# Kernel optimization log

Measured on AMD Instinct MI355X. Metric: run time of the kernel, lower is better.

## Reference

```python
import jax, jax.numpy as jnp
import numpy as np

D_MODEL = 768
D_INNER = 1536
D_STATE = 16
D_CONV = 4
DT_RANK = 48
N_LAYER = 4
VOCAB = 32000
B, L = 2, 1024


def rmsnorm(x, w, eps=1e-5):
    return x * jax.lax.rsqrt(jnp.mean(x * x, axis=-1, keepdims=True) + eps) * w


def depthwise_causal_conv(u, w):
    # u: (b, l, d_in), w: (d_in, k). torch pads both sides then truncates to l,
    # which equals left-pad by k-1 (causal).
    b, l, d = u.shape
    k = w.shape[1]
    up = jnp.pad(u, ((0, 0), (k - 1, 0), (0, 0)))
    out = jnp.zeros_like(u)
    for i in range(k):
        out = out + up[:, i:i + l, :] * w[:, i]
    return out


def selective_scan(u, delta, A, Bm, C, Dp):
    # u,delta: (b,l,d_in); A: (d_in,n); Bm,C: (b,l,n); Dp: (d_in,)
    dA = jnp.exp(delta[..., None] * A)                      # (b,l,d,n)
    dBu = delta[..., None] * Bm[:, :, None, :] * u[..., None]

    def step(h, inp):
        dA_t, dBu_t, C_t = inp
        h = dA_t * h + dBu_t                                 # (b,d,n)
        y = jnp.einsum('bdn,bn->bd', h, C_t)
        return h, y

    h0 = jnp.zeros_like(dA[:, 0])
    xs = (jnp.moveaxis(dA, 1, 0), jnp.moveaxis(dBu, 1, 0), jnp.moveaxis(C, 1, 0))
    _, ys = jax.lax.scan(step, h0, xs)                       # (l,b,d)
    return jnp.moveaxis(ys, 0, 1) + u * Dp


def setup_inputs() -> dict:
    key = jax.random.key(0)
    ks = jax.random.split(key, 16)
    s = lambda fan: 1.0 / np.sqrt(fan)
    inp = {}
    inp['text_input'] = jax.random.randint(ks[0], (B, L), 0, VOCAB)
    inp['visual_input'] = jax.random.normal(ks[1], (B, L, D_MODEL), dtype=jnp.float32)
    inp['embedding'] = jax.random.normal(ks[2], (VOCAB, D_MODEL), dtype=jnp.float32) * 0.02
    inp['norm_w'] = jnp.ones((N_LAYER, D_MODEL), dtype=jnp.float32)
    inp['norm_f_w'] = jnp.ones((D_MODEL,), dtype=jnp.float32)
    inp['in_proj_w'] = jax.random.normal(ks[3], (N_LAYER, 2 * D_INNER, D_MODEL)) * s(D_MODEL)
    inp['in_proj2_w'] = jax.random.normal(ks[4], (N_LAYER, D_INNER, D_MODEL)) * s(D_MODEL)
    inp['conv_w'] = jax.random.normal(ks[5], (N_LAYER, D_INNER, D_CONV)) * s(D_CONV)
    inp['conv_b'] = jax.random.normal(ks[6], (N_LAYER, D_INNER)) * 0.01
    inp['x_proj_w'] = jax.random.normal(ks[7], (N_LAYER, DT_RANK + D_STATE, D_INNER)) * s(D_INNER)
    inp['c_proj_w'] = jax.random.normal(ks[8], (N_LAYER, D_STATE, D_INNER)) * s(D_INNER)
    inp['dt_proj_w'] = jax.random.normal(ks[9], (N_LAYER, D_INNER, DT_RANK)) * s(DT_RANK)
    inp['dt_proj_b'] = jax.random.normal(ks[10], (N_LAYER, D_INNER)) * 0.01
    A = jnp.tile(jnp.arange(1, D_STATE + 1, dtype=jnp.float32)[None, :], (D_INNER, 1))
    inp['A_log'] = jnp.tile(jnp.log(A)[None], (N_LAYER, 1, 1))
    inp['D'] = jnp.ones((N_LAYER, D_INNER), dtype=jnp.float32)
    inp['out_proj_w'] = jax.random.normal(ks[11], (N_LAYER, D_MODEL, D_INNER)) * s(D_INNER)
    return inp


def reference(text_input, visual_input, embedding, norm_w, norm_f_w, in_proj_w,
              in_proj2_w, conv_w, conv_b, x_proj_w, c_proj_w, dt_proj_w,
              dt_proj_b, A_log, D, out_proj_w):
    x = embedding[text_input]  # (b,l,d_model)
    n_layer = A_log.shape[0]
    l = x.shape[1]
    for i in range(n_layer):
        q = rmsnorm(x, norm_w[i])
        v = rmsnorm(visual_input, norm_w[i])
        xr = q @ in_proj_w[i].T                               # (b,l,2*d_inner)
        vin = v @ in_proj2_w[i].T                             # (b,l,d_inner)
        t, res = jnp.split(xr, 2, axis=-1)
        t = depthwise_causal_conv(t, conv_w[i]) + conv_b[i]
        t = jax.nn.silu(t)
        # ssm
        A = -jnp.exp(A_log[i])
        x_dbl = t @ x_proj_w[i].T                             # (b,l,dt_rank+n)
        delta, Bm = jnp.split(x_dbl, [DT_RANK], axis=-1)
        C = vin @ c_proj_w[i].T                               # (b,l,n)
        delta = jax.nn.softplus(delta @ dt_proj_w[i].T + dt_proj_b[i])
        y = selective_scan(t, delta, A, Bm, C, D[i])
        y = y * jax.nn.silu(res)
        x = y @ out_proj_w[i].T + x
    x = rmsnorm(x, norm_f_w)
    return x @ embedding.T  # tied lm_head -> (b,l,vocab)
```

## Files before the change

### kernel.cpp

```cpp
#include <hip/hip_runtime.h>
#include <hip/hip_bf16.h>
#include <math.h>

#define B_ 2
#define L_ 1024
#define DM 768
#define DI 1536
#define DS 16
#define DR 48
#define NL 4
#define VOC 32000
#define BL (B_*L_)
#define NCH 32
#define LCH (L_/NCH)
#define NXD 80
#define DTILE 8

typedef __attribute__((ext_vector_type(8))) short short8;
typedef __attribute__((ext_vector_type(4))) float f32x4;

__device__ __forceinline__ float sigmoidf_(float x){ return 1.f/(1.f+expf(-x)); }
__device__ __forceinline__ float siluf_(float x){ return x*sigmoidf_(x); }
__device__ __forceinline__ float softplusf_(float x){ return fmaxf(x,0.f) + log1pf(expf(-fabsf(x))); }
__device__ __forceinline__ unsigned short f2bf(float f){
    unsigned u = __float_as_uint(f);
    u += 0x7FFFu + ((u >> 16) & 1u);
    return (unsigned short)(u >> 16);
}
__device__ __forceinline__ float bf2f(unsigned short h){
    return __uint_as_float((unsigned)h << 16);
}
__device__ __forceinline__ void gload_lds16(const unsigned short* g, unsigned short* l){
    __builtin_amdgcn_global_load_lds(
        (const __attribute__((address_space(1))) void*)g,
        (__attribute__((address_space(3))) void*)l, 16, 0, 0);
}

__global__ void cast_bf16_kernel(const float* __restrict__ in, unsigned short* __restrict__ out, int n4)
{
    for (int i = blockIdx.x*256 + threadIdx.x; i < n4; i += gridDim.x*256) {
        float4 v = ((const float4*)in)[i];
        ushort4 o;
        o.x = f2bf(v.x); o.y = f2bf(v.y); o.z = f2bf(v.z); o.w = f2bf(v.w);
        ((ushort4*)out)[i] = o;
    }
}

__global__ void embed_kernel(const int* __restrict__ idx, const float* __restrict__ emb,
                             float* __restrict__ x)
{
    int i = blockIdx.x*256 + threadIdx.x;
    if (i >= BL*DM) return;
    int c = i % DM; int bl = i / DM;
    x[i] = emb[(size_t)idx[bl]*DM + c];
}

__global__ void rmsnorm_bf_kernel(const float* __restrict__ in, const float* __restrict__ w,
                                  unsigned short* __restrict__ out)
{
    int row = blockIdx.x;
    const float* xr = in + (size_t)row*DM;
    float ss = 0.f;
    for (int c = threadIdx.x; c < DM; c += 256) { float v = xr[c]; ss += v*v; }
    #pragma unroll
    for (int o = 32; o > 0; o >>= 1) ss += __shfl_down(ss, o, 64);
    __shared__ float red[4];
    if ((threadIdx.x & 63) == 0) red[threadIdx.x >> 6] = ss;
    __syncthreads();
    float tot = red[0] + red[1] + red[2] + red[3];
    float scale = rsqrtf(tot * (1.f/DM) + 1e-5f);
    for (int c = threadIdx.x; c < DM; c += 256)
        out[(size_t)row*DM + c] = f2bf(xr[c]*scale*w[c]);
}

__global__ void prep_layer(
    const float* __restrict__ x, const float* __restrict__ vis, const float* __restrict__ w,
    unsigned short* __restrict__ qh, unsigned short* __restrict__ ql,
    unsigned short* __restrict__ vh, unsigned short* __restrict__ vl,
    const float* __restrict__ s1, unsigned short* __restrict__ h1, unsigned short* __restrict__ l1, int n1,
    const float* __restrict__ s2, unsigned short* __restrict__ h2, unsigned short* __restrict__ l2, int n2,
    const float* __restrict__ s3, unsigned short* __restrict__ h3, unsigned short* __restrict__ l3, int n3)
{
    if (blockIdx.x < 2*BL) {
        int row = blockIdx.x;
        bool first = row < BL;
        int r = first ? row : row - BL;
        const float* xr = (first ? x : vis) + (size_t)r*DM;
        unsigned short* oh = (first ? qh : vh) + (size_t)r*DM;
        unsigned short* ol = (first ? ql : vl) + (size_t)r*DM;
        float ss = 0.f;
        for (int c = threadIdx.x; c < DM; c += 256) { float v = xr[c]; ss += v*v; }
        #pragma unroll
        for (int o = 32; o > 0; o >>= 1) ss += __shfl_down(ss, o, 64);
        __shared__ float red[4];
        if ((threadIdx.x & 63) == 0) red[threadIdx.x >> 6] = ss;
        __syncthreads();
        float tot = red[0] + red[1] + red[2] + red[3];
        float scale = rsqrtf(tot * (1.f/DM) + 1e-5f);
        for (int c = threadIdx.x; c < DM; c += 256) {
            float v = xr[c]*scale*w[c];
            unsigned short h = f2bf(v);
            oh[c] = h;
            ol[c] = f2bf(v - bf2f(h));
        }
    } else {
        int total = n1 + n2 + n3;
        int nblk = gridDim.x - 2*BL;
        for (int i = (blockIdx.x - 2*BL)*256 + threadIdx.x; i < total; i += nblk*256) {
            const float* s; unsigned short *h, *l; int j;
            if (i < n1)           { s = s1; h = h1; l = l1; j = i; }
            else if (i < n1 + n2) { s = s2; h = h2; l = l2; j = i - n1; }
            else                  { s = s3; h = h3; l = l3; j = i - n1 - n2; }
            float4 v = ((const float4*)s)[j];
            ushort4 hh, ll;
            hh.x = f2bf(v.x); ll.x = f2bf(v.x - bf2f(hh.x));
            hh.y = f2bf(v.y); ll.y = f2bf(v.y - bf2f(hh.y));
            hh.z = f2bf(v.z); ll.z = f2bf(v.z - bf2f(hh.z));
            hh.w = f2bf(v.w); ll.w = f2bf(v.w - bf2f(hh.w));
            ((ushort4*)h)[j] = hh;
            ((ushort4*)l)[j] = ll;
        }
    }
}

__global__ __launch_bounds__(256) void gemm_head(
    const unsigned short* __restrict__ A, int lda,
    const unsigned short* __restrict__ W, int ldb,
    float* __restrict__ C, int ldc, int K)
{
    __shared__ unsigned short As[128*64];
    __shared__ unsigned short Bs[128*64];
    const int tid = threadIdx.x;
    const int bm = blockIdx.y*128, bn = blockIdx.x*128;
    const int l  = tid & 63;
    const int w  = tid >> 6;
    const int wr = (w >> 1)*64, wc = (w & 1)*64;
    const int lr = l & 15, lg = l >> 4;

    f32x4 zero4 = {0.f, 0.f, 0.f, 0.f};
    f32x4 acc[4][4];
    #pragma unroll
    for (int m = 0; m < 4; m++)
        #pragma unroll
        for (int n = 0; n < 4; n++) acc[m][n] = zero4;

    for (int k0 = 0; k0 < K; k0 += 64) {
        __syncthreads();
        #pragma unroll
        for (int i = 0; i < 4; i++) {
            int c   = i*256 + tid;
            int row = c >> 3;
            int kb  = c & 7;
            int kbs = (kb ^ (row & 7)) << 3;
            gload_lds16(A + (size_t)(bm+row)*lda + k0 + kbs, &As[c*8]);
            gload_lds16(W + (size_t)(bn+row)*ldb + k0 + kbs, &Bs[c*8]);
        }
        __syncthreads();
        #pragma unroll
        for (int kk = 0; kk < 2; kk++) {
            short8 af[4], bfr[4];
            #pragma unroll
            for (int m = 0; m < 4; m++) {
                int row = wr + m*16 + lr;
                af[m] = *(const short8*)&As[row*64 + (((kk*4+lg) ^ (row & 7)) << 3)];
            }
            #pragma unroll
            for (int n = 0; n < 4; n++) {
                int row = wc + n*16 + lr;
                bfr[n] = *(const short8*)&Bs[row*64 + (((kk*4+lg) ^ (row & 7)) << 3)];
            }
            #pragma unroll
            for (int m = 0; m < 4; m++)
                #pragma unroll
                for (int n = 0; n < 4; n++)
                    acc[m][n] = __builtin_amdgcn_mfma_f32_16x16x32_bf16(af[m], bfr[n], acc[m][n], 0, 0, 0);
        }
    }

    #pragma unroll
    for (int m = 0; m < 4; m++)
        #pragma unroll
        for (int n = 0; n < 4; n++) {
            int col = bn + wc + n*16 + lr;
            #pragma unroll
            for (int r = 0; r < 4; r++) {
                int rowi = bm + wr + m*16 + lg*4 + r;
                C[(size_t)rowi*ldc + col] = acc[m][n][r];
            }
        }
}

template<int EPI>
__device__ __forceinline__ void mfma2_body(
    const unsigned short* __restrict__ Ah, const unsigned short* __restrict__ Alo, int lda,
    const unsigned short* __restrict__ Wh, const unsigned short* __restrict__ Wlo, int ldb,
    float* __restrict__ C, int ldc, const float* __restrict__ extra,
    int K, int bm, int bn,
    unsigned short* Ash, unsigned short* Asl, unsigned short* Bsh, unsigned short* Bsl)
{
    const int tid = threadIdx.x;
    const int l  = tid & 63;
    const int w  = tid >> 6;
    const int wr = (w >> 1)*64, wc = (w & 1)*64;
    const int lr = l & 15, lg = l >> 4;

    f32x4 zero4 = {0.f, 0.f, 0.f, 0.f};
    f32x4 acc[4][4];
    #pragma unroll
    for (int m = 0; m < 4; m++)
        #pragma unroll
        for (int n = 0; n < 4; n++) acc[m][n] = zero4;

    for (int k0 = 0; k0 < K; k0 += 64) {
        __syncthreads();
        #pragma unroll
        for (int i = 0; i < 4; i++) {
            int c   = i*256 + tid;
            int row = c >> 3;
            int kb  = c & 7;
            int kbs = (kb ^ (row & 7)) << 3;
            const size_t ao = (size_t)(bm+row)*lda + k0 + kbs;
            const size_t bo = (size_t)(bn+row)*ldb + k0 + kbs;
            gload_lds16(Ah  + ao, &Ash[c*8]);
            gload_lds16(Alo + ao, &Asl[c*8]);
            gload_lds16(Wh  + bo, &Bsh[c*8]);
            gload_lds16(Wlo + bo, &Bsl[c*8]);
        }
        __syncthreads();
        #pragma unroll
        for (int kk = 0; kk < 2; kk++) {
            short8 ah[4], al[4], bh[4], bl[4];
            #pragma unroll
            for (int m = 0; m < 4; m++) {
                int row = wr + m*16 + lr;
                int so  = row*64 + (((kk*4 + lg) ^ (row & 7)) << 3);
                ah[m] = *(const short8*)&Ash[so];
                al[m] = *(const short8*)&Asl[so];
            }
            #pragma unroll
            for (int n = 0; n < 4; n++) {
                int row = wc + n*16 + lr;
                int so  = row*64 + (((kk*4 + lg) ^ (row & 7)) << 3);
                bh[n] = *(const short8*)&Bsh[so];
                bl[n] = *(const short8*)&Bsl[so];
            }
            #pragma unroll
            for (int m = 0; m < 4; m++)
                #pragma unroll
                for (int n = 0; n < 4; n++) {
                    acc[m][n] = __builtin_amdgcn_mfma_f32_16x16x32_bf16(al[m], bh[n], acc[m][n], 0, 0, 0);
                    acc[m][n] = __builtin_amdgcn_mfma_f32_16x16x32_bf16(ah[m], bl[n], acc[m][n], 0, 0, 0);
                    acc[m][n] = __builtin_amdgcn_mfma_f32_16x16x32_bf16(ah[m], bh[n], acc[m][n], 0, 0, 0);
                }
        }
    }

    #pragma unroll
    for (int m = 0; m < 4; m++)
        #pragma unroll
        for (int n = 0; n < 4; n++) {
            int col = bn + wc + n*16 + lr;
            #pragma unroll
            for (int r = 0; r < 4; r++) {
                int rowi = bm + wr + m*16 + lg*4 + r;
                float v = acc[m][n][r];
                if (EPI == 1) v += extra[(size_t)rowi*ldc + col];
                C[(size_t)rowi*ldc + col] = v;
            }
        }
}

template<int EPI>
__global__ __launch_bounds__(256) void gemm_mfma2(
    const unsigned short* __restrict__ Ah, const unsigned short* __restrict__ Alo, int lda,
    const unsigned short* __restrict__ Wh, const unsigned short* __restrict__ Wlo, int ldb,
    float* __restrict__ C, int ldc, const float* __restrict__ extra, int K)
{
    __shared__ unsigned short Ash[128*64];
    __shared__ unsigned short Asl[128*64];
    __shared__ unsigned short Bsh[128*64];
    __shared__ unsigned short Bsl[128*64];
    mfma2_body<EPI>(Ah, Alo, lda, Wh, Wlo, ldb, C, ldc, extra, K,
                    blockIdx.y*128, blockIdx.x*128, Ash, Asl, Bsh, Bsl);
}

__global__ __launch_bounds__(256) void gemm_mfma2_dual(
    const unsigned short* __restrict__ Ah1, const unsigned short* __restrict__ Al1,
    const unsigned short* __restrict__ Wh1, const unsigned short* __restrict__ Wl1,
    float* __restrict__ C1, int ldc1, int nb1,
    const unsigned short* __restrict__ Ah2, const unsigned short* __restrict__ Al2,
    const unsigned short* __restrict__ Wh2, const unsigned short* __restrict__ Wl2,
    float* __restrict__ C2, int ldc2,
    int lda, int ldb, int K)
{
    __shared__ unsigned short Ash[128*64];
    __shared__ unsigned short Asl[128*64];
    __shared__ unsigned short Bsh[128*64];
    __shared__ unsigned short Bsl[128*64];
    int bx = blockIdx.x;
    if (bx < nb1)
        mfma2_body<0>(Ah1, Al1, lda, Wh1, Wl1, ldb, C1, ldc1, nullptr, K,
                      blockIdx.y*128, bx*128, Ash, Asl, Bsh, Bsl);
    else
        mfma2_body<0>(Ah2, Al2, lda, Wh2, Wl2, ldb, C2, ldc2, nullptr, K,
                      blockIdx.y*128, (bx-nb1)*128, Ash, Asl, Bsh, Bsl);
}

template<int EPI>
__global__ __launch_bounds__(256) void gemm_tile(
    const float* __restrict__ A, int lda,
    const float* __restrict__ W, int ldb,
    float* __restrict__ C, int ldc,
    const float* __restrict__ extra,
    int K)
{
    __shared__ float As[8][128];
    __shared__ float Bs[8][128];
    const int bm = blockIdx.y * 128;
    const int bn = blockIdx.x * 128;
    const int tid = threadIdx.x;
    const int lr = tid >> 1;
    const int lh = (tid & 1) * 4;
    const int tr = tid >> 4;
    const int tc = tid & 15;

    float acc[8][8];
    #pragma unroll
    for (int i = 0; i < 8; i++)
        #pragma unroll
        for (int j = 0; j < 8; j++) acc[i][j] = 0.f;

    const float* Arow = A + (size_t)(bm + lr)*lda + lh;
    const float* Wrow = W + (size_t)(bn + lr)*ldb + lh;

    for (int k0 = 0; k0 < K; k0 += 8) {
        float4 av = *(const float4*)(Arow + k0);
        float4 wv = *(const float4*)(Wrow + k0);
        __syncthreads();
        As[lh+0][lr] = av.x; As[lh+1][lr] = av.y; As[lh+2][lr] = av.z; As[lh+3][lr] = av.w;
        Bs[lh+0][lr] = wv.x; Bs[lh+1][lr] = wv.y; Bs[lh+2][lr] = wv.z; Bs[lh+3][lr] = wv.w;
        __syncthreads();
        #pragma unroll
        for (int k = 0; k < 8; k++) {
            float a[8], b[8];
            *(float4*)(a)   = *(const float4*)&As[k][tr*8];
            *(float4*)(a+4) = *(const float4*)&As[k][tr*8+4];
            *(float4*)(b)   = *(const float4*)&Bs[k][tc*8];
            *(float4*)(b+4) = *(const float4*)&Bs[k][tc*8+4];
            #pragma unroll
            for (int i = 0; i < 8; i++)
                #pragma unroll
                for (int j = 0; j < 8; j++)
                    acc[i][j] = fmaf(a[i], b[j], acc[i][j]);
        }
    }

    #pragma unroll
    for (int i = 0; i < 8; i++) {
        int row = bm + tr*8 + i;
        float* crow = C + (size_t)row*ldc + bn + tc*8;
        float v[8];
        if (EPI == 2) {
            const float* bia = extra + bn + tc*8;
            #pragma unroll
            for (int j = 0; j < 8; j++) v[j] = softplusf_(acc[i][j] + bia[j]);
        } else {
            #pragma unroll
            for (int j = 0; j < 8; j++) v[j] = acc[i][j];
        }
        *(float4*)(crow)   = make_float4(v[0],v[1],v[2],v[3]);
        *(float4*)(crow+4) = make_float4(v[4],v[5],v[6],v[7]);
    }
}

__global__ __launch_bounds__(256) void gemm_skinny2(
    const float* __restrict__ A1, const float* __restrict__ A2, int lda,
    const float* __restrict__ W1, const float* __restrict__ W2, int ldb,
    float* __restrict__ outx, int K)
{
    __shared__ float As[64][36];
    __shared__ float Ws[16][36];
    int tid = threadIdx.x;
    int bx = blockIdx.x;
    bool isC = (bx == 4);
    const float* A = isC ? A2 : A1;
    const float* W = isC ? W2 : W1;
    int bn = isC ? 0 : bx*16;
    int colbase = isC ? 64 : bx*16;
    int bm = blockIdx.y*64;
    int ar = tid >> 2, ak = (tid & 3)*8;
    int wr = tid >> 4, wk = (tid & 15)*2;
    int tr = tid >> 4, tc = tid & 15;

    float acc[4] = {0.f,0.f,0.f,0.f};
    for (int k0 = 0; k0 < K; k0 += 32) {
        float4 a0 = *(const float4*)(A + (size_t)(bm+ar)*lda + k0 + ak);
        float4 a1 = *(const float4*)(A + (size_t)(bm+ar)*lda + k0 + ak + 4);
        float2 wv = *(const float2*)(W + (size_t)(bn+wr)*ldb + k0 + wk);
        __syncthreads();
        *(float4*)&As[ar][ak]   = a0;
        *(float4*)&As[ar][ak+4] = a1;
        Ws[wr][wk] = wv.x; Ws[wr][wk+1] = wv.y;
        __syncthreads();
        #pragma unroll
        for (int k = 0; k < 32; k += 4) {
            float4 wv4 = *(const float4*)&Ws[tc][k];
            #pragma unroll
            for (int i = 0; i < 4; i++) {
                float4 av4 = *(const float4*)&As[tr*4+i][k];
                acc[i] = fmaf(av4.x, wv4.x, acc[i]);
                acc[i] = fmaf(av4.y, wv4.y, acc[i]);
                acc[i] = fmaf(av4.z, wv4.z, acc[i]);
                acc[i] = fmaf(av4.w, wv4.w, acc[i]);
            }
        }
    }
    #pragma unroll
    for (int i = 0; i < 4; i++)
        outx[(size_t)(bm + tr*4 + i)*NXD + colbase + tc] = acc[i];
}

__global__ void conv_silu_kernel(const float* __restrict__ xr, const float* __restrict__ cw,
                                 const float* __restrict__ cb, float* __restrict__ t)
{
    int i = blockIdx.x*256 + threadIdx.x;
    if (i >= BL*DI) return;
    int d = i % DI; int bl = i / DI; int l = bl % L_; int b = bl / L_;
    const float* base = xr + (size_t)b*L_*(2*DI);
    float acc = cb[d];
    #pragma unroll
    for (int q = 0; q < 4; q++) {
        int ll = l - 3 + q;
        if (ll >= 0) acc = fmaf(base[(size_t)ll*(2*DI) + d], cw[d*4+q], acc);
    }
    t[i] = siluf_(acc);
}

__global__ __launch_bounds__(256) void scan_fused(
    const float* __restrict__ delta, const float* __restrict__ t,
    const float* __restrict__ xdbl,
    const float* __restrict__ A_log, const float* __restrict__ Dp,
    const float* __restrict__ xr,
    unsigned short* __restrict__ zh, unsigned short* __restrict__ zl)
{
    __shared__ float P_lds[256*17];
    __shared__ float S_lds[256*17];
    int blk = blockIdx.x;
    int b  = blk / (DI/DTILE);
    int d0 = (blk % (DI/DTILE))*DTILE;
    int tid = threadIdx.x;
    int dl = tid & 7, c = tid >> 3;
    int d = d0 + dl;

    float Ad[16];
    #pragma unroll
    for (int n = 0; n < 16; n++) Ad[n] = -expf(A_log[d*16+n]);

    float P[16], S[16];
    #pragma unroll
    for (int n = 0; n < 16; n++) { P[n] = 1.f; S[n] = 0.f; }
    for (int s = 0; s < LCH; s++) {
        int bl = b*L_ + c*LCH + s;
        float dt = delta[(size_t)bl*DI + d];
        float u  = t[(size_t)bl*DI + d];
        const float4* Bp4 = (const float4*)(xdbl + (size_t)bl*NXD + 48);
        float Bv[16];
        #pragma unroll
        for (int q = 0; q < 4; q++) {
            float4 bv = Bp4[q];
            Bv[q*4+0]=bv.x; Bv[q*4+1]=bv.y; Bv[q*4+2]=bv.z; Bv[q*4+3]=bv.w;
        }
        float du = dt*u;
        #pragma unroll
        for (int n = 0; n < 16; n++) {
            float a = expf(dt*Ad[n]);
            P[n] *= a;
            S[n] = fmaf(a, S[n], du*Bv[n]);
        }
    }
    #pragma unroll
    for (int n = 0; n < 16; n++) { P_lds[tid*17+n] = P[n]; S_lds[tid*17+n] = S[n]; }
    __syncthreads();

    if (tid < 128) {
        int dl2 = tid >> 4, n2 = tid & 15;
        float h = 0.f;
        for (int cc = 0; cc < NCH; cc++) {
            int slot = cc*8 + dl2;
            float p = P_lds[slot*17 + n2];
            float s = S_lds[slot*17 + n2];
            S_lds[slot*17 + n2] = h;
            h = fmaf(p, h, s);
        }
    }
    __syncthreads();

    float h[16];
    #pragma unroll
    for (int n = 0; n < 16; n++) h[n] = S_lds[tid*17+n];
    float Dd = Dp[d];
    for (int s = 0; s < LCH; s++) {
        int bl = b*L_ + c*LCH + s;
        float dt = delta[(size_t)bl*DI + d];
        float u  = t[(size_t)bl*DI + d];
        const float4* Bp4 = (const float4*)(xdbl + (size_t)bl*NXD + 48);
        const float4* Cp4 = (const float4*)(xdbl + (size_t)bl*NXD + 64);
        float Bv[16], Cv[16];
        #pragma unroll
        for (int q = 0; q < 4; q++) {
            float4 bv = Bp4[q]; float4 cv = Cp4[q];
            Bv[q*4+0]=bv.x; Bv[q*4+1]=bv.y; Bv[q*4+2]=bv.z; Bv[q*4+3]=bv.w;
            Cv[q*4+0]=cv.x; Cv[q*4+1]=cv.y; Cv[q*4+2]=cv.z; Cv[q*4+3]=cv.w;
        }
        float du = dt*u;
        float y = 0.f;
        #pragma unroll
        for (int n = 0; n < 16; n++) {
            float a = expf(dt*Ad[n]);
            h[n] = fmaf(a, h[n], du*Bv[n]);
            y = fmaf(h[n], Cv[n], y);
        }
        y = fmaf(u, Dd, y);
        float r = xr[(size_t)bl*(2*DI) + DI + d];
        float zv = y * siluf_(r);
        unsigned short hh = f2bf(zv);
        zh[(size_t)bl*DI + d] = hh;
        zl[(size_t)bl*DI + d] = f2bf(zv - bf2f(hh));
    }
}

extern "C" void kernel_launch(void* const* d_in, const int* in_sizes, int n_in,
                              void* d_out, int out_size, void* d_ws, size_t ws_size,
                              hipStream_t stream)
{
    const int*   text     = (const int*)  d_in[0];
    const float* visual   = (const float*)d_in[1];
    const float* emb      = (const float*)d_in[2];
    const float* norm_w   = (const float*)d_in[3];
    const float* norm_f_w = (const float*)d_in[4];
    const float* in_proj  = (const float*)d_in[5];
    const float* in_proj2 = (const float*)d_in[6];
    const float* conv_w   = (const float*)d_in[7];
    const float* conv_b   = (const float*)d_in[8];
    const float* x_proj   = (const float*)d_in[9];
    const float* c_proj   = (const float*)d_in[10];
    const float* dt_w     = (const float*)d_in[11];
    const float* dt_b     = (const float*)d_in[12];
    const float* A_log    = (const float*)d_in[13];
    const float* Dp       = (const float*)d_in[14];
    const float* out_proj = (const float*)d_in[15];
    float* out = (float*)d_out;

    float* ws = (float*)d_ws;
    size_t off = 0;
    float* x     = ws + off; off += (size_t)BL*DM;
    float* xr    = ws + off; off += (size_t)BL*2*DI;
    float* vin   = ws + off; off += (size_t)BL*DI;
    float* tb    = ws + off; off += (size_t)BL*DI;
    float* dl    = ws + off; off += (size_t)BL*DI;
    float* xdbl  = ws + off; off += (size_t)BL*NXD;

    unsigned short* bfb = (unsigned short*)(ws + off);
    size_t bo = 0;
    unsigned short* emb_bf = bfb + bo; bo += (size_t)VOC*DM;
    unsigned short* wA_h   = bfb + bo; bo += (size_t)2*DI*DM;
    unsigned short* wA_l   = bfb + bo; bo += (size_t)2*DI*DM;
    unsigned short* wB_h   = bfb + bo; bo += (size_t)DI*DM;
    unsigned short* wB_l   = bfb + bo; bo += (size_t)DI*DM;
    unsigned short* wO_h   = bfb + bo; bo += (size_t)DM*DI;
    unsigned short* wO_l   = bfb + bo; bo += (size_t)DM*DI;
    unsigned short* q_h    = bfb + bo; bo += (size_t)BL*DM;
    unsigned short* q_l    = bfb + bo; bo += (size_t)BL*DM;
    unsigned short* v_h    = bfb + bo; bo += (size_t)BL*DM;
    unsigned short* v_l    = bfb + bo; bo += (size_t)BL*DM;
    unsigned short* z_h    = bfb + bo; bo += (size_t)BL*DI;
    unsigned short* z_l    = bfb + bo; bo += (size_t)BL*DI;
    unsigned short* xn_bf  = bfb + bo; bo += (size_t)BL*DM;

    dim3 blk(256);

    cast_bf16_kernel<<<dim3(2048), blk, 0, stream>>>(emb, emb_bf, VOC*DM/4);

    embed_kernel<<<dim3((BL*DM)/256), blk, 0, stream>>>(text, emb, x);

    for (int i = 0; i < NL; i++) {
        const float* nw = norm_w + (size_t)i*DM;

        prep_layer<<<dim3(2*BL + 1024), blk, 0, stream>>>(
            x, visual, nw, q_h, q_l, v_h, v_l,
            in_proj  + (size_t)i*2*DI*DM, wA_h, wA_l, 2*DI*DM/4,
            in_proj2 + (size_t)i*DI*DM,   wB_h, wB_l, DI*DM/4,
            out_proj + (size_t)i*DM*DI,   wO_h, wO_l, DM*DI/4);

        gemm_mfma2_dual<<<dim3(2*DI/128 + DI/128, BL/128), blk, 0, stream>>>(
            q_h, q_l, wA_h, wA_l, xr, 2*DI, 2*DI/128,
            v_h, v_l, wB_h, wB_l, vin, DI,
            DM, DM, DM);

        conv_silu_kernel<<<dim3((BL*DI)/256), blk, 0, stream>>>(
            xr, conv_w + (size_t)i*DI*4, conv_b + (size_t)i*DI, tb);

        gemm_skinny2<<<dim3(5, BL/64), blk, 0, stream>>>(
            tb, vin, DI, x_proj + (size_t)i*(DR+DS)*DI, c_proj + (size_t)i*DS*DI, DI,
            xdbl, DI);

        gemm_tile<2><<<dim3(DI/128, BL/128), blk, 0, stream>>>(
            xdbl, NXD, dt_w + (size_t)i*DI*DR, DR, dl, DI, dt_b + (size_t)i*DI, DR);

        scan_fused<<<dim3(B_*DI/DTILE), blk, 0, stream>>>(
            dl, tb, xdbl, A_log + (size_t)i*DI*DS, Dp + (size_t)i*DI, xr, z_h, z_l);

        gemm_mfma2<1><<<dim3(DM/128, BL/128), blk, 0, stream>>>(
            z_h, z_l, DI, wO_h, wO_l, DI, x, DM, x, DI);
    }

    rmsnorm_bf_kernel<<<dim3(BL), blk, 0, stream>>>(x, norm_f_w, xn_bf);
    gemm_head<<<dim3(VOC/128, BL/128), blk, 0, stream>>>(
        xn_bf, DM, emb_bf, DM, out, VOC, DM);
}
```

Measured before the change: 1.587 ms.

## Split-K out_proj GEMM with residual reduce; finer scan chunking

The out_proj GEMM is now split along K into four slices, each writing to its own partial buffer, and a separate reduction kernel sums the partials and adds them into the residual. This raises the grid from 96 blocks to 384 so the device's compute units are better filled. The scan kernel now uses 64 chunks over 4 channels per block instead of 32 chunks over 8 channels, which doubles the block count and halves the serial length per thread. In exchange it adds an extra kernel launch, the write and read of partial buffers, and a longer serial cross-chunk combine per block.

```diff
diff --git a/kernel.cpp b/kernel.cpp
--- a/kernel.cpp
+++ b/kernel.cpp
@@ -11,10 +11,10 @@
 #define NL 4
 #define VOC 32000
 #define BL (B_*L_)
-#define NCH 32
+#define NCH 64
 #define LCH (L_/NCH)
 #define NXD 80
-#define DTILE 8
+#define DTILE 4
 
 typedef __attribute__((ext_vector_type(8))) short short8;
 typedef __attribute__((ext_vector_type(4))) float f32x4;
@@ -270,18 +270,37 @@
         }
 }
 
-template<int EPI>
-__global__ __launch_bounds__(256) void gemm_mfma2(
+__global__ __launch_bounds__(256) void gemm_mfma2_splitk(
     const unsigned short* __restrict__ Ah, const unsigned short* __restrict__ Alo, int lda,
     const unsigned short* __restrict__ Wh, const unsigned short* __restrict__ Wlo, int ldb,
-    float* __restrict__ C, int ldc, const float* __restrict__ extra, int K)
+    float* __restrict__ partial, int ldc, int kslice)
 {
     __shared__ unsigned short Ash[128*64];
     __shared__ unsigned short Asl[128*64];
     __shared__ unsigned short Bsh[128*64];
     __shared__ unsigned short Bsl[128*64];
-    mfma2_body<EPI>(Ah, Alo, lda, Wh, Wlo, ldb, C, ldc, extra, K,
-                    blockIdx.y*128, blockIdx.x*128, Ash, Asl, Bsh, Bsl);
+    int z = blockIdx.z;
+    int ko = z*kslice;
+    mfma2_body<0>(Ah + ko, Alo + ko, lda, Wh + ko, Wlo + ko, ldb,
+                  partial + (size_t)z*BL*DM, ldc, nullptr, kslice,
+                  blockIdx.y*128, blockIdx.x*128, Ash, Asl, Bsh, Bsl);
+}
+
+__global__ void reduce4_res(const float* __restrict__ partial, float* __restrict__ x, int n4)
+{
+    const int MN4 = n4;
+    for (int i = blockIdx.x*256 + threadIdx.x; i < n4; i += gridDim.x*256) {
+        float4 p0 = ((const float4*)partial)[i];
+        float4 p1 = ((const float4*)partial)[i + MN4];
+        float4 p2 = ((const float4*)partial)[i + 2*MN4];
+        float4 p3 = ((const float4*)partial)[i + 3*MN4];
+        float4 xv = ((float4*)x)[i];
+        xv.x += p0.x + p1.x + p2.x + p3.x;
+        xv.y += p0.y + p1.y + p2.y + p3.y;
+        xv.z += p0.z + p1.z + p2.z + p3.z;
+        xv.w += p0.w + p1.w + p2.w + p3.w;
+        ((float4*)x)[i] = xv;
+    }
 }
 
 __global__ __launch_bounds__(256) void gemm_mfma2_dual(
@@ -449,7 +468,7 @@
     int b  = blk / (DI/DTILE);
     int d0 = (blk % (DI/DTILE))*DTILE;
     int tid = threadIdx.x;
-    int dl = tid & 7, c = tid >> 3;
+    int dl = tid & (DTILE-1), c = tid >> 2;
     int d = d0 + dl;
 
     float Ad[16];
@@ -482,11 +501,11 @@
     for (int n = 0; n < 16; n++) { P_lds[tid*17+n] = P[n]; S_lds[tid*17+n] = S[n]; }
     __syncthreads();
 
-    if (tid < 128) {
+    if (tid < DTILE*16) {
         int dl2 = tid >> 4, n2 = tid & 15;
         float h = 0.f;
         for (int cc = 0; cc < NCH; cc++) {
-            int slot = cc*8 + dl2;
+            int slot = cc*DTILE + dl2;
             float p = P_lds[slot*17 + n2];
             float s = S_lds[slot*17 + n2];
             S_lds[slot*17 + n2] = h;
@@ -559,6 +578,7 @@
     float* tb    = ws + off; off += (size_t)BL*DI;
     float* dl    = ws + off; off += (size_t)BL*DI;
     float* xdbl  = ws + off; off += (size_t)BL*NXD;
+    float* part  = ws + off; off += (size_t)4*BL*DM;
 
     unsigned short* bfb = (unsigned short*)(ws + off);
     size_t bo = 0;
@@ -610,8 +630,9 @@
         scan_fused<<<dim3(B_*DI/DTILE), blk, 0, stream>>>(
             dl, tb, xdbl, A_log + (size_t)i*DI*DS, Dp + (size_t)i*DI, xr, z_h, z_l);
 
-        gemm_mfma2<1><<<dim3(DM/128, BL/128), blk, 0, stream>>>(
-            z_h, z_l, DI, wO_h, wO_l, DI, x, DM, x, DI);
+        gemm_mfma2_splitk<<<dim3(DM/128, BL/128, 4), blk, 0, stream>>>(
+            z_h, z_l, DI, wO_h, wO_l, DI, part, DM, DI/4);
+        reduce4_res<<<dim3(1536), blk, 0, stream>>>(part, x, BL*DM/4);
     }
 
     rmsnorm_bf_kernel<<<dim3(BL), blk, 0, stream>>>(x, norm_f_w, xn_bf);
```

New measurement: 1.611 ms. About the same (+1.6%).

## Rewrite LM head GEMM with 256x256 tiles, 8 waves and double-buffered LDS

Applied to the files above, without the earlier changes.

Replaces the 128x128, 4-wave LM head GEMM with a 256x256 tile using 512 threads. Global-to-LDS loads are double-buffered with explicit vmcnt waits, so the next K tile loads while MFMAs run, and s_setprio raises priority around the MFMA issue. The larger tile raises data reuse, at the cost of 128KB of LDS per block, more accumulator registers, and fewer blocks (125x8). The scan kernel edits only parameterise constants on DTILE.

```diff
diff --git a/kernel.cpp b/kernel.cpp
--- a/kernel.cpp
+++ b/kernel.cpp
@@ -123,68 +123,91 @@
     }
 }
 
-__global__ __launch_bounds__(256) void gemm_head(
+__global__ __launch_bounds__(512) void gemm_head8(
     const unsigned short* __restrict__ A, int lda,
     const unsigned short* __restrict__ W, int ldb,
     float* __restrict__ C, int ldc, int K)
 {
-    __shared__ unsigned short As[128*64];
-    __shared__ unsigned short Bs[128*64];
+    __shared__ unsigned short As[2][256*64];
+    __shared__ unsigned short Bs[2][256*64];
     const int tid = threadIdx.x;
-    const int bm = blockIdx.y*128, bn = blockIdx.x*128;
+    const int bm = blockIdx.y*256, bn = blockIdx.x*256;
     const int l  = tid & 63;
     const int w  = tid >> 6;
-    const int wr = (w >> 1)*64, wc = (w & 1)*64;
+    const int wm = w >> 2, wn = w & 3;
     const int lr = l & 15, lg = l >> 4;
 
+    auto stage = [&](int t, int db) {
+        int k0 = t*64;
+        #pragma unroll
+        for (int i = 0; i < 4; i++) {
+            int c = i*512 + tid;
+            int row = c >> 3, kb = c & 7;
+            int kbs = (kb ^ (row & 7)) << 3;
+            gload_lds16(A + (size_t)(bm+row)*lda + k0 + kbs, &As[db][c*8]);
+        }
+        #pragma unroll
+        for (int i = 0; i < 4; i++) {
+            int c = i*512 + tid;
+            int row = c >> 3, kb = c & 7;
+            int kbs = (kb ^ (row & 7)) << 3;
+            gload_lds16(W + (size_t)(bn+row)*ldb + k0 + kbs, &Bs[db][c*8]);
+        }
+    };
+
     f32x4 zero4 = {0.f, 0.f, 0.f, 0.f};
-    f32x4 acc[4][4];
-    #pragma unroll
-    for (int m = 0; m < 4; m++)
+    f32x4 acc[8][4];
+    #pragma unroll
+    for (int m = 0; m < 8; m++)
         #pragma unroll
         for (int n = 0; n < 4; n++) acc[m][n] = zero4;
 
-    for (int k0 = 0; k0 < K; k0 += 64) {
-        __syncthreads();
-        #pragma unroll
-        for (int i = 0; i < 4; i++) {
-            int c   = i*256 + tid;
-            int row = c >> 3;
-            int kb  = c & 7;
-            int kbs = (kb ^ (row & 7)) << 3;
-            gload_lds16(A + (size_t)(bm+row)*lda + k0 + kbs, &As[c*8]);
-            gload_lds16(W + (size_t)(bn+row)*ldb + k0 + kbs, &Bs[c*8]);
-        }
-        __syncthreads();
-        #pragma unroll
-        for (int kk = 0; kk < 2; kk++) {
-            short8 af[4], bfr[4];
-            #pragma unroll
-            for (int m = 0; m < 4; m++) {
-                int row = wr + m*16 + lr;
-                af[m] = *(const short8*)&As[row*64 + (((kk*4+lg) ^ (row & 7)) << 3)];
+    const int NT = K/64;
+    stage(0, 0);
+    stage(1, 1);
+
+    for (int t = 0; t < NT; t++) {
+        int cur = t & 1;
+        if (t + 1 < NT) { asm volatile("s_waitcnt vmcnt(8)" ::: "memory"); }
+        else            { asm volatile("s_waitcnt vmcnt(0)" ::: "memory"); }
+        __builtin_amdgcn_s_barrier();
+        __builtin_amdgcn_sched_barrier(0);
+
+        const unsigned short* Ab = As[cur];
+        const unsigned short* Bb = Bs[cur];
+        short8 bf0[4], bf1[4];
+        #pragma unroll
+        for (int n = 0; n < 4; n++) {
+            int row = wn*64 + n*16 + lr;
+            bf0[n] = *(const short8*)&Bb[row*64 + ((lg       ^ (row & 7)) << 3)];
+            bf1[n] = *(const short8*)&Bb[row*64 + (((4 + lg) ^ (row & 7)) << 3)];
+        }
+        #pragma unroll
+        for (int m = 0; m < 8; m++) {
+            int row = wm*128 + m*16 + lr;
+            short8 a0 = *(const short8*)&Ab[row*64 + ((lg       ^ (row & 7)) << 3)];
+            short8 a1 = *(const short8*)&Ab[row*64 + (((4 + lg) ^ (row & 7)) << 3)];
+            __builtin_amdgcn_s_setprio(1);
+            #pragma unroll
+            for (int n = 0; n < 4; n++) {
+                acc[m][n] = __builtin_amdgcn_mfma_f32_16x16x32_bf16(a0, bf0[n], acc[m][n], 0, 0, 0);
+                acc[m][n] = __builtin_amdgcn_mfma_f32_16x16x32_bf16(a1, bf1[n], acc[m][n], 0, 0, 0);
             }
-            #pragma unroll
-            for (int n = 0; n < 4; n++) {
-                int row = wc + n*16 + lr;
-                bfr[n] = *(const short8*)&Bs[row*64 + (((kk*4+lg) ^ (row & 7)) << 3)];
-            }
-            #pragma unroll
-            for (int m = 0; m < 4; m++)
-                #pragma unroll
-                for (int n = 0; n < 4; n++)
-                    acc[m][n] = __builtin_amdgcn_mfma_f32_16x16x32_bf16(af[m], bfr[n], acc[m][n], 0, 0, 0);
-        }
-    }
-
-    #pragma unroll
-    for (int m = 0; m < 4; m++)
+            __builtin_amdgcn_s_setprio(0);
+        }
+        __builtin_amdgcn_sched_barrier(0);
+        __builtin_amdgcn_s_barrier();
+        if (t + 2 < NT) stage(t + 2, cur);
+    }
+
+    #pragma unroll
+    for (int m = 0; m < 8; m++)
         #pragma unroll
         for (int n = 0; n < 4; n++) {
-            int col = bn + wc + n*16 + lr;
+            int col = bn + wn*64 + n*16 + lr;
             #pragma unroll
             for (int r = 0; r < 4; r++) {
-                int rowi = bm + wr + m*16 + lg*4 + r;
+                int rowi = bm + wm*128 + m*16 + lg*4 + r;
                 C[(size_t)rowi*ldc + col] = acc[m][n][r];
             }
         }
@@ -449,7 +472,7 @@
     int b  = blk / (DI/DTILE);
     int d0 = (blk % (DI/DTILE))*DTILE;
     int tid = threadIdx.x;
-    int dl = tid & 7, c = tid >> 3;
+    int dl = tid & (DTILE-1), c = tid / DTILE;
     int d = d0 + dl;
 
     float Ad[16];
@@ -482,11 +505,11 @@
     for (int n = 0; n < 16; n++) { P_lds[tid*17+n] = P[n]; S_lds[tid*17+n] = S[n]; }
     __syncthreads();
 
-    if (tid < 128) {
+    if (tid < DTILE*16) {
         int dl2 = tid >> 4, n2 = tid & 15;
         float h = 0.f;
         for (int cc = 0; cc < NCH; cc++) {
-            int slot = cc*8 + dl2;
+            int slot = cc*DTILE + dl2;
             float p = P_lds[slot*17 + n2];
             float s = S_lds[slot*17 + n2];
             S_lds[slot*17 + n2] = h;
@@ -615,6 +638,6 @@
     }
 
     rmsnorm_bf_kernel<<<dim3(BL), blk, 0, stream>>>(x, norm_f_w, xn_bf);
-    gemm_head<<<dim3(VOC/128, BL/128), blk, 0, stream>>>(
+    gemm_head8<<<dim3(VOC/256, BL/256), dim3(512), 0, stream>>>(
         xn_bf, DM, emb_bf, DM, out, VOC, DM);
 }
```

After: 1.588 ms. No clear change (+0.1%).
